# Performance work log

Measured on AMD Instinct MI355X. Metric: run time of the kernel, lower is better.

## Reference

```python
import jax, jax.numpy as jnp
import numpy as np

N_HEADS = 16


def setup_inputs() -> dict:
    key = jax.random.key(0)
    k1, k2, k3 = jax.random.split(key, 3)
    b, t, d = 2, 2048, 1024
    x = jax.random.normal(k1, (b, t, d), dtype=jnp.float32)
    # nn.Linear weights (stored here as [in, out]); 0.02 scale ~ standard init
    w_qkv = jax.random.normal(k2, (d, 3 * d), dtype=jnp.float32) * 0.02
    w_out = jax.random.normal(k3, (d, d), dtype=jnp.float32) * 0.02
    return {"x": x, "w_qkv": w_qkv, "w_out": w_out}


def reference(x, w_qkv, w_out):
    # Causal multi-head self-attention. The original module implements this
    # via a hand-rolled blockwise flash-attention loop with online softmax;
    # the intended math is exactly standard causal SDPA, expressed densely here.
    b, t, d = x.shape
    h = N_HEADS
    hd = d // h
    qkv = (x @ w_qkv).reshape(b, t, 3, h, hd)
    qkv = jnp.transpose(qkv, (2, 0, 3, 1, 4))  # [3, b, h, t, hd]
    q, k, v = qkv[0], qkv[1], qkv[2]
    scale = 1.0 / jnp.sqrt(jnp.float32(hd))
    s = jnp.einsum("bhqd,bhkd->bhqk", q, k) * scale  # [b, h, t, t]
    causal = jnp.tril(jnp.ones((t, t), dtype=bool))
    s = jnp.where(causal, s, -jnp.inf)
    p = jax.nn.softmax(s, axis=-1)
    o = jnp.einsum("bhqk,bhkd->bhqd", p, v)
    o = jnp.transpose(o, (0, 2, 1, 3)).reshape(b, t, d)
    return o @ w_out
```

## Files before the change

kernel.cpp:

```cpp
#include <hip/hip_runtime.h>

typedef float f32x4 __attribute__((ext_vector_type(4)));
typedef float f32x16 __attribute__((ext_vector_type(16)));
typedef short short8 __attribute__((ext_vector_type(8)));
typedef short short4_t __attribute__((ext_vector_type(4)));

#define GLOAD_LDS16(gp, lp) \
  __builtin_amdgcn_global_load_lds((const __attribute__((address_space(1))) void*)(gp), \
                                   (__attribute__((address_space(3))) void*)(lp), 16, 0, 0)

__device__ __forceinline__ short f2bf(float f){
  unsigned u = __builtin_bit_cast(unsigned, f);
  u += 0x7fffu + ((u >> 16) & 1u);
  return (short)(u >> 16);
}

__device__ __forceinline__ float exp2_fast(float x){
  return __builtin_amdgcn_exp2f(x);
}

__global__ void cvt_kernel(const float* __restrict__ x, short* __restrict__ xb, int n4){
  for (int i = blockIdx.x*blockDim.x + threadIdx.x; i < n4; i += gridDim.x*blockDim.x){
    f32x4 v = ((const f32x4*)x)[i];
    short4_t s;
    s[0]=f2bf(v[0]); s[1]=f2bf(v[1]); s[2]=f2bf(v[2]); s[3]=f2bf(v[3]);
    ((short4_t*)xb)[i] = s;
  }
}

__global__ __launch_bounds__(256) void transpose_cvt_kernel(const float* __restrict__ w,
                                                            short* __restrict__ wT,
                                                            int K, int N){
  __shared__ float tile[32][33];
  int bn = blockIdx.x*32, bk = blockIdx.y*32;
  int tx = threadIdx.x & 31, ty = threadIdx.x >> 5;
  #pragma unroll
  for (int r=ty; r<32; r+=8) tile[r][tx] = w[(size_t)(bk+r)*N + bn + tx];
  __syncthreads();
  #pragma unroll
  for (int r=ty; r<32; r+=8) wT[(size_t)(bn+r)*K + bk + tx] = f2bf(tile[tx][r]);
}

template<int MODE>
__global__ __launch_bounds__(256) void gemm128_kernel(
    const short* __restrict__ A, const short* __restrict__ Bt,
    float* __restrict__ Cf, short* __restrict__ qb_, short* __restrict__ kb_,
    short* __restrict__ vtb, int M, int N, int K)
{
  __shared__ short a_lds[128*64];
  __shared__ short b_lds[128*64];
  const int tid = threadIdx.x;
  const int lane = tid & 63;
  const int l15 = lane & 15, lg = lane >> 4;
  const int w  = tid >> 6;
  const int wr = w >> 1, wc = w & 1;
  const int m0 = blockIdx.x * 128, n0 = blockIdx.y * 128;

  f32x4 acc[4][4];
  #pragma unroll
  for (int i=0;i<4;i++)
    #pragma unroll
    for (int j=0;j<4;j++) acc[i][j] = (f32x4){0.f,0.f,0.f,0.f};

  for (int kt = 0; kt < K; kt += 64){
    __syncthreads();
    #pragma unroll
    for (int i=0;i<4;i++){
      int u = i*256 + tid;
      int row = u >> 3, cu = u & 7;
      int kl = ((cu ^ (row & 7)) << 3);
      GLOAD_LDS16(A + (size_t)(m0+row)*K + kt + kl, a_lds + (size_t)(i*256 + (tid & ~63))*8);
    }
    #pragma unroll
    for (int i=0;i<4;i++){
      int u = i*256 + tid;
      int row = u >> 3, cu = u & 7;
      int kl = ((cu ^ (row & 7)) << 3);
      GLOAD_LDS16(Bt + (size_t)(n0+row)*K + kt + kl, b_lds + (size_t)(i*256 + (tid & ~63))*8);
    }
    asm volatile("s_waitcnt vmcnt(0)" ::: "memory");
    __syncthreads();

    #pragma unroll
    for (int kk=0;kk<2;kk++){
      short8 af[4], bfr[4];
      #pragma unroll
      for (int mi=0;mi<4;mi++){
        int row = wr*64 + mi*16 + l15;
        int uu = ((kk*4 + lg) ^ (row & 7));
        af[mi] = *(const short8*)&a_lds[row*64 + uu*8];
      }
      #pragma unroll
      for (int ni=0;ni<4;ni++){
        int row = wc*64 + ni*16 + l15;
        int uu = ((kk*4 + lg) ^ (row & 7));
        bfr[ni] = *(const short8*)&b_lds[row*64 + uu*8];
      }
      #pragma unroll
      for (int mi=0;mi<4;mi++)
        #pragma unroll
        for (int ni=0;ni<4;ni++)
          acc[mi][ni] = __builtin_amdgcn_mfma_f32_16x16x32_bf16(af[mi], bfr[ni], acc[mi][ni], 0,0,0);
    }
  }

  #pragma unroll
  for (int mi=0;mi<4;mi++){
    #pragma unroll
    for (int ni=0;ni<4;ni++){
      int col = n0 + wc*64 + ni*16 + l15;
      #pragma unroll
      for (int r=0;r<4;r++){
        int rowg = m0 + wr*64 + mi*16 + lg*4 + r;
        float v = acc[mi][ni][r];
        if (MODE == 0){
          Cf[(size_t)rowg*N + col] = v;
        } else {
          int three = col >> 10, hh = (col >> 6) & 15, e = col & 63;
          int bb = rowg >> 11, t = rowg & 2047;
          int bh = bb*16 + hh;
          if (three == 0)      qb_[((size_t)bh*2048 + t)*64 + e] = f2bf(v * (0.125f*1.44269504f));
          else if (three == 1) kb_[((size_t)bh*2048 + t)*64 + e] = f2bf(v);
          else                 vtb[((size_t)bh*64 + e)*2048 + t] = f2bf(v);
        }
      }
    }
  }
}

__global__ __launch_bounds__(256) void attn_kernel(
    const short* __restrict__ q, const short* __restrict__ kbuf,
    const short* __restrict__ vt, short* __restrict__ ob)
{
  __shared__ short k_lds[2][128*64];
  __shared__ short v_lds[2][64*128];

  const int tid = threadIdx.x, lane = tid & 63, w = tid >> 6;
  const int l31 = lane & 31, hi = lane >> 5;
  const int qi = blockIdx.x >> 5;
  const int qb = (qi < 8) ? (15 - qi) : (qi - 8);
  const int bh = blockIdx.x & 31;
  const int q0 = qb * 128;

  const short* qg = q + ((size_t)bh*2048 + q0 + w*32 + l31)*64 + hi*8;
  short8 qf[4];
  #pragma unroll
  for (int kk=0;kk<4;kk++) qf[kk] = *(const short8*)(qg + kk*16);

  f32x16 o_acc[2];
  #pragma unroll
  for (int oc=0;oc<2;oc++)
    #pragma unroll
    for (int r=0;r<16;r++) o_acc[oc][r] = 0.f;
  float mreg = -1e30f, lreg = 0.f;

  const int sw = l31 & 7;
  int kro[4], vro[8];
  #pragma unroll
  for (int kk=0;kk<4;kk++) kro[kk] = l31*128 + (((kk*2+hi)^sw) << 4);
  #pragma unroll
  for (int ks=0;ks<8;ks++) vro[ks] = l31*256 + (((ks*2+hi)^sw) << 4);

  const int xk = ((tid & 7) ^ ((tid >> 3) & 7)) * 8;
  const int xv = ((tid & 15) ^ ((tid >> 4) & 7)) * 8;
  const short* kp = kbuf + (size_t)bh*2048*64 + (size_t)(tid >> 3)*64 + xk;
  const short* vp = vt   + (size_t)bh*64*2048 + (size_t)(tid >> 4)*2048 + xv;
  const int dst = (tid & ~63)*8;

  const int n = qb + 1;
  #pragma unroll
  for (int i=0;i<4;i++) GLOAD_LDS16(kp + i*2048,  &k_lds[0][i*2048 + dst]);
  #pragma unroll
  for (int i=0;i<4;i++) GLOAD_LDS16(vp + i*32768, &v_lds[0][i*2048 + dst]);
  kp += 8192; vp += 128;

  for (int s = 0; s < n; s++){
    const int cur = s & 1;
    if (s + 1 < n){
      #pragma unroll
      for (int i=0;i<4;i++) GLOAD_LDS16(kp + i*2048,  &k_lds[cur^1][i*2048 + dst]);
      #pragma unroll
      for (int i=0;i<4;i++) GLOAD_LDS16(vp + i*32768, &v_lds[cur^1][i*2048 + dst]);
      kp += 8192; vp += 128;
      asm volatile("s_waitcnt vmcnt(8)" ::: "memory");
    } else {
      asm volatile("s_waitcnt vmcnt(0)" ::: "memory");
    }
    __builtin_amdgcn_s_barrier();

    const char* kl_ = (const char*)&k_lds[cur][0];
    const char* vl_ = (const char*)&v_lds[cur][0];

    f32x16 sacc[4];
    #pragma unroll
    for (int ct=0;ct<4;ct++)
      #pragma unroll
      for (int r=0;r<16;r++) sacc[ct][r] = 0.f;
    __builtin_amdgcn_s_setprio(1);
    #pragma unroll
    for (int kk=0;kk<4;kk++){
      #pragma unroll
      for (int ct=0;ct<4;ct++){
        short8 kf = *(const short8*)(kl_ + kro[kk] + ct*4096);
        sacc[ct] = __builtin_amdgcn_mfma_f32_32x32x16_bf16(kf, qf[kk], sacc[ct], 0,0,0);
      }
    }
    __builtin_amdgcn_s_setprio(0);

    if (s == qb){
      const int qloc = w*32 + l31 - 4*hi;
      #pragma unroll
      for (int ct=0;ct<4;ct++)
        #pragma unroll
        for (int r=0;r<16;r++)
          if (ct*32 + (r&3) + 8*(r>>2) > qloc) sacc[ct][r] = -1e30f;
    }

    float pmax = sacc[0][0];
    #pragma unroll
    for (int ct=0;ct<4;ct++)
      #pragma unroll
      for (int r=0;r<16;r++) pmax = fmaxf(pmax, sacc[ct][r]);
    pmax = fmaxf(pmax, __shfl_xor(pmax, 32));

    if (!__all(pmax - mreg <= 8.0f)){
      float mnew = fmaxf(mreg, pmax);
      float alpha = exp2_fast(mreg - mnew);
      mreg = mnew;
      lreg *= alpha;
      float aRow[16];
      #pragma unroll
      for (int r=0;r<16;r++) aRow[r] = __shfl(alpha, (r&3) + 8*(r>>2) + 4*hi);
      #pragma unroll
      for (int oc=0;oc<2;oc++)
        #pragma unroll
        for (int r=0;r<16;r++) o_acc[oc][r] *= aRow[r];
    }

    float sum = 0.f;
    #pragma unroll
    for (int ct=0;ct<4;ct++){
      float pv[16];
      #pragma unroll
      for (int r=0;r<16;r++){ pv[r] = exp2_fast(sacc[ct][r] - mreg); sum += pv[r]; }
      unsigned pk[8];
      #pragma unroll
      for (int t=0;t<8;t++)
        asm("v_cvt_pk_bf16_f32 %0, %1, %2" : "=v"(pk[t]) : "v"(pv[2*t]), "v"(pv[2*t+1]));
      #pragma unroll
      for (int kss=0;kss<2;kss++){
        const int W = 4*kss;
        unsigned x0 = pk[W],   x2 = pk[W+2];
        unsigned x1 = pk[W+1], x3 = pk[W+3];
        asm("v_permlane32_swap_b32 %0, %1" : "+v"(x0), "+v"(x2));
        asm("v_permlane32_swap_b32 %0, %1" : "+v"(x1), "+v"(x3));
        uint4 pau = {x0, x1, x2, x3};
        short8 pa = __builtin_bit_cast(short8, pau);
        __builtin_amdgcn_s_setprio(1);
        #pragma unroll
        for (int oc=0;oc<2;oc++){
          short8 vf = *(const short8*)(vl_ + vro[2*ct+kss] + oc*8192);
          o_acc[oc] = __builtin_amdgcn_mfma_f32_32x32x16_bf16(pa, vf, o_acc[oc], 0,0,0);
        }
        __builtin_amdgcn_s_setprio(0);
      }
    }
    sum += __shfl_xor(sum, 32);
    lreg += sum;

    __builtin_amdgcn_s_barrier();
  }

  const int bb = bh >> 4, hh = bh & 15;
  #pragma unroll
  for (int r=0;r<16;r++){
    float lf = __shfl(lreg, (r&3) + 8*(r>>2) + 4*hi);
    float inv = 1.0f / lf;
    int t = q0 + w*32 + (r&3) + 8*(r>>2) + 4*hi;
    size_t base = ((size_t)(bb*2048 + t))*1024 + (size_t)hh*64 + l31;
    ob[base]      = f2bf(o_acc[0][r] * inv);
    ob[base + 32] = f2bf(o_acc[1][r] * inv);
  }
}

extern "C" void kernel_launch(void* const* d_in, const int* in_sizes, int n_in,
                              void* d_out, int out_size, void* d_ws, size_t ws_size,
                              hipStream_t stream) {
  const float* x     = (const float*)d_in[0];
  const float* w_qkv = (const float*)d_in[1];
  const float* w_out = (const float*)d_in[2];
  float* out = (float*)d_out;

  char* ws = (char*)d_ws;
  short* xb    = (short*)(ws);
  short* wqkvT = (short*)(ws + (8u  << 20));
  short* woutT = (short*)(ws + (14u << 20));
  short* qbuf  = (short*)(ws + (16u << 20));
  short* kbuf  = (short*)(ws + (24u << 20));
  short* vtbuf = (short*)(ws + (32u << 20));
  short* obuf  = (short*)(ws + (40u << 20));

  cvt_kernel<<<2048, 256, 0, stream>>>(x, xb, (4096*1024)/4);
  transpose_cvt_kernel<<<dim3(96,32), 256, 0, stream>>>(w_qkv, wqkvT, 1024, 3072);
  transpose_cvt_kernel<<<dim3(32,32), 256, 0, stream>>>(w_out, woutT, 1024, 1024);

  gemm128_kernel<1><<<dim3(32,24), 256, 0, stream>>>(xb, wqkvT, nullptr,
                                                     qbuf, kbuf, vtbuf, 4096, 3072, 1024);
  attn_kernel<<<dim3(512), 256, 0, stream>>>(qbuf, kbuf, vtbuf, obuf);
  gemm128_kernel<0><<<dim3(32,8), 256, 0, stream>>>(obuf, woutT, out,
                                                    nullptr, nullptr, nullptr, 4096, 1024, 1024);
}
```

Before: 117.2 us.

## Shrink attention KV tile from 128 to 64 keys and batch PV MFMAs

The flash-attention kernel now streams K and V in 64-key tiles instead of 128, halving LDS per buffer and doubling loop iterations. The causal mask applies to the last two tiles. PV MFMAs are deferred until all P fragments are built. Smaller LDS may allow more resident blocks per CU, and the diagonal tile does less masked work, at the cost of twice as many barriers and more per-iteration softmax overhead.

```diff
diff --git a/kernel.cpp b/kernel.cpp
--- a/kernel.cpp
+++ b/kernel.cpp
@@ -132,8 +132,8 @@
     const short* __restrict__ q, const short* __restrict__ kbuf,
     const short* __restrict__ vt, short* __restrict__ ob)
 {
-  __shared__ short k_lds[2][128*64];
-  __shared__ short v_lds[2][64*128];
+  __shared__ short k_lds[2][64*64];
+  __shared__ short v_lds[2][64*64];
 
   const int tid = threadIdx.x, lane = tid & 63, w = tid >> 6;
   const int l31 = lane & 31, hi = lane >> 5;
@@ -155,34 +155,31 @@
   float mreg = -1e30f, lreg = 0.f;
 
   const int sw = l31 & 7;
-  int kro[4], vro[8];
-  #pragma unroll
-  for (int kk=0;kk<4;kk++) kro[kk] = l31*128 + (((kk*2+hi)^sw) << 4);
-  #pragma unroll
-  for (int ks=0;ks<8;ks++) vro[ks] = l31*256 + (((ks*2+hi)^sw) << 4);
-
-  const int xk = ((tid & 7) ^ ((tid >> 3) & 7)) * 8;
-  const int xv = ((tid & 15) ^ ((tid >> 4) & 7)) * 8;
-  const short* kp = kbuf + (size_t)bh*2048*64 + (size_t)(tid >> 3)*64 + xk;
-  const short* vp = vt   + (size_t)bh*64*2048 + (size_t)(tid >> 4)*2048 + xv;
+  int ro[4];
+  #pragma unroll
+  for (int u=0;u<4;u++) ro[u] = l31*128 + (((u*2+hi)^sw) << 4);
+
+  const int xsw = ((tid & 7) ^ ((tid >> 3) & 7)) * 8;
+  const short* kp = kbuf + (size_t)bh*2048*64 + (size_t)(tid >> 3)*64   + xsw;
+  const short* vp = vt   + (size_t)bh*64*2048 + (size_t)(tid >> 3)*2048 + xsw;
   const int dst = (tid & ~63)*8;
 
-  const int n = qb + 1;
-  #pragma unroll
-  for (int i=0;i<4;i++) GLOAD_LDS16(kp + i*2048,  &k_lds[0][i*2048 + dst]);
-  #pragma unroll
-  for (int i=0;i<4;i++) GLOAD_LDS16(vp + i*32768, &v_lds[0][i*2048 + dst]);
-  kp += 8192; vp += 128;
+  const int n = 2*qb + 2;
+  #pragma unroll
+  for (int i=0;i<2;i++) GLOAD_LDS16(kp + i*2048,  &k_lds[0][i*2048 + dst]);
+  #pragma unroll
+  for (int i=0;i<2;i++) GLOAD_LDS16(vp + i*65536, &v_lds[0][i*2048 + dst]);
+  kp += 4096; vp += 64;
 
   for (int s = 0; s < n; s++){
     const int cur = s & 1;
     if (s + 1 < n){
       #pragma unroll
-      for (int i=0;i<4;i++) GLOAD_LDS16(kp + i*2048,  &k_lds[cur^1][i*2048 + dst]);
-      #pragma unroll
-      for (int i=0;i<4;i++) GLOAD_LDS16(vp + i*32768, &v_lds[cur^1][i*2048 + dst]);
-      kp += 8192; vp += 128;
-      asm volatile("s_waitcnt vmcnt(8)" ::: "memory");
+      for (int i=0;i<2;i++) GLOAD_LDS16(kp + i*2048,  &k_lds[cur^1][i*2048 + dst]);
+      #pragma unroll
+      for (int i=0;i<2;i++) GLOAD_LDS16(vp + i*65536, &v_lds[cur^1][i*2048 + dst]);
+      kp += 4096; vp += 64;
+      asm volatile("s_waitcnt vmcnt(4)" ::: "memory");
     } else {
       asm volatile("s_waitcnt vmcnt(0)" ::: "memory");
     }
@@ -191,34 +188,35 @@
     const char* kl_ = (const char*)&k_lds[cur][0];
     const char* vl_ = (const char*)&v_lds[cur][0];
 
-    f32x16 sacc[4];
-    #pragma unroll
-    for (int ct=0;ct<4;ct++)
+    f32x16 sacc[2];
+    #pragma unroll
+    for (int ct=0;ct<2;ct++)
       #pragma unroll
       for (int r=0;r<16;r++) sacc[ct][r] = 0.f;
     __builtin_amdgcn_s_setprio(1);
     #pragma unroll
     for (int kk=0;kk<4;kk++){
       #pragma unroll
-      for (int ct=0;ct<4;ct++){
-        short8 kf = *(const short8*)(kl_ + kro[kk] + ct*4096);
+      for (int ct=0;ct<2;ct++){
+        short8 kf = *(const short8*)(kl_ + ro[kk] + ct*4096);
         sacc[ct] = __builtin_amdgcn_mfma_f32_32x32x16_bf16(kf, qf[kk], sacc[ct], 0,0,0);
       }
     }
     __builtin_amdgcn_s_setprio(0);
 
-    if (s == qb){
+    if (s >= 2*qb){
+      const int d = s - 2*qb;
       const int qloc = w*32 + l31 - 4*hi;
       #pragma unroll
-      for (int ct=0;ct<4;ct++)
+      for (int ct=0;ct<2;ct++)
         #pragma unroll
         for (int r=0;r<16;r++)
-          if (ct*32 + (r&3) + 8*(r>>2) > qloc) sacc[ct][r] = -1e30f;
+          if (d*64 + ct*32 + (r&3) + 8*(r>>2) > qloc) sacc[ct][r] = -1e30f;
     }
 
     float pmax = sacc[0][0];
     #pragma unroll
-    for (int ct=0;ct<4;ct++)
+    for (int ct=0;ct<2;ct++)
       #pragma unroll
       for (int r=0;r<16;r++) pmax = fmaxf(pmax, sacc[ct][r]);
     pmax = fmaxf(pmax, __shfl_xor(pmax, 32));
@@ -238,8 +236,9 @@
     }
 
     float sum = 0.f;
-    #pragma unroll
-    for (int ct=0;ct<4;ct++){
+    short8 pa[4];
+    #pragma unroll
+    for (int ct=0;ct<2;ct++){
       float pv[16];
       #pragma unroll
       for (int r=0;r<16;r++){ pv[r] = exp2_fast(sacc[ct][r] - mreg); sum += pv[r]; }
@@ -255,18 +254,22 @@
         asm("v_permlane32_swap_b32 %0, %1" : "+v"(x0), "+v"(x2));
         asm("v_permlane32_swap_b32 %0, %1" : "+v"(x1), "+v"(x3));
         uint4 pau = {x0, x1, x2, x3};
-        short8 pa = __builtin_bit_cast(short8, pau);
-        __builtin_amdgcn_s_setprio(1);
-        #pragma unroll
-        for (int oc=0;oc<2;oc++){
-          short8 vf = *(const short8*)(vl_ + vro[2*ct+kss] + oc*8192);
-          o_acc[oc] = __builtin_amdgcn_mfma_f32_32x32x16_bf16(pa, vf, o_acc[oc], 0,0,0);
-        }
-        __builtin_amdgcn_s_setprio(0);
+        pa[2*ct+kss] = __builtin_bit_cast(short8, pau);
       }
     }
     sum += __shfl_xor(sum, 32);
     lreg += sum;
+
+    __builtin_amdgcn_s_setprio(1);
+    #pragma unroll
+    for (int ks=0;ks<4;ks++){
+      #pragma unroll
+      for (int oc=0;oc<2;oc++){
+        short8 vf = *(const short8*)(vl_ + ro[ks] + oc*4096);
+        o_acc[oc] = __builtin_amdgcn_mfma_f32_32x32x16_bf16(pa[ks], vf, o_acc[oc], 0,0,0);
+      }
+    }
+    __builtin_amdgcn_s_setprio(0);
 
     __builtin_amdgcn_s_barrier();
   }
```

Measured after the change: 124.2 us. +6.0%, slower.

## Merge prep conversions into one kernel and transpose V in a separate pass

Applied to the files above, without the earlier changes.

Fuses the x conversion and both weight transpose-conversions into a single launch that dispatches on block index. The QKV GEMM now writes V in row-major [bh,t,e] layout, and a new LDS-based transpose kernel produces V^T for attention. This replaces the GEMM epilogue's strided scatter into V^T with coalesced stores. In exchange it adds an extra launch and an extra read and write of V, and the output buffer reuses the V buffer region.

```diff
diff --git a/kernel.cpp b/kernel.cpp
--- a/kernel.cpp
+++ b/kernel.cpp
@@ -19,21 +19,31 @@
   return __builtin_amdgcn_exp2f(x);
 }
 
-__global__ void cvt_kernel(const float* __restrict__ x, short* __restrict__ xb, int n4){
-  for (int i = blockIdx.x*blockDim.x + threadIdx.x; i < n4; i += gridDim.x*blockDim.x){
-    f32x4 v = ((const f32x4*)x)[i];
-    short4_t s;
-    s[0]=f2bf(v[0]); s[1]=f2bf(v[1]); s[2]=f2bf(v[2]); s[3]=f2bf(v[3]);
-    ((short4_t*)xb)[i] = s;
-  }
-}
-
-__global__ __launch_bounds__(256) void transpose_cvt_kernel(const float* __restrict__ w,
-                                                            short* __restrict__ wT,
-                                                            int K, int N){
+__global__ __launch_bounds__(256) void prep_kernel(
+    const float* __restrict__ x, const float* __restrict__ wqkv,
+    const float* __restrict__ wout, short* __restrict__ xb,
+    short* __restrict__ wqkvT, short* __restrict__ woutT)
+{
   __shared__ float tile[32][33];
-  int bn = blockIdx.x*32, bk = blockIdx.y*32;
-  int tx = threadIdx.x & 31, ty = threadIdx.x >> 5;
+  const int bid = blockIdx.x, tid = threadIdx.x;
+  if (bid < 512){
+    int base = bid*2048 + tid;
+    #pragma unroll
+    for (int it=0; it<8; it++){
+      int i = base + it*256;
+      f32x4 v = ((const f32x4*)x)[i];
+      short4_t s;
+      s[0]=f2bf(v[0]); s[1]=f2bf(v[1]); s[2]=f2bf(v[2]); s[3]=f2bf(v[3]);
+      ((short4_t*)xb)[i] = s;
+    }
+    return;
+  }
+  const float* w; short* wT; int N, idx;
+  if (bid < 3584){ w = wqkv; wT = wqkvT; N = 3072; idx = bid - 512;  }
+  else           { w = wout; wT = woutT; N = 1024; idx = bid - 3584; }
+  const int K = 1024;
+  int bn = (idx % (N >> 5)) * 32, bk = (idx / (N >> 5)) * 32;
+  int tx = tid & 31, ty = tid >> 5;
   #pragma unroll
   for (int r=ty; r<32; r+=8) tile[r][tx] = w[(size_t)(bk+r)*N + bn + tx];
   __syncthreads();
@@ -45,7 +55,7 @@
 __global__ __launch_bounds__(256) void gemm128_kernel(
     const short* __restrict__ A, const short* __restrict__ Bt,
     float* __restrict__ Cf, short* __restrict__ qb_, short* __restrict__ kb_,
-    short* __restrict__ vtb, int M, int N, int K)
+    short* __restrict__ vb_, int M, int N, int K)
 {
   __shared__ short a_lds[128*64];
   __shared__ short b_lds[128*64];
@@ -121,11 +131,34 @@
           int bh = bb*16 + hh;
           if (three == 0)      qb_[((size_t)bh*2048 + t)*64 + e] = f2bf(v * (0.125f*1.44269504f));
           else if (three == 1) kb_[((size_t)bh*2048 + t)*64 + e] = f2bf(v);
-          else                 vtb[((size_t)bh*64 + e)*2048 + t] = f2bf(v);
+          else                 vb_[((size_t)bh*2048 + t)*64 + e] = f2bf(v);
         }
       }
     }
   }
+}
+
+__global__ __launch_bounds__(256) void transpose_v_kernel(const short* __restrict__ vb,
+                                                          short* __restrict__ vtb){
+  __shared__ short tl[64][66];
+  const int bh = blockIdx.x >> 5, t0 = (blockIdx.x & 31)*64;
+  const int r = threadIdx.x >> 2, c4 = (threadIdx.x & 3)*16;
+  const short* src = vb + ((size_t)bh*2048 + t0 + r)*64 + c4;
+  short8 a0 = *(const short8*)(src);
+  short8 a1 = *(const short8*)(src + 8);
+  #pragma unroll
+  for (int j=0;j<8;j++) tl[r][c4+j] = a0[j];
+  #pragma unroll
+  for (int j=0;j<8;j++) tl[r][c4+8+j] = a1[j];
+  __syncthreads();
+  short8 b0, b1;
+  #pragma unroll
+  for (int j=0;j<8;j++) b0[j] = tl[c4+j][r];
+  #pragma unroll
+  for (int j=0;j<8;j++) b1[j] = tl[c4+8+j][r];
+  short* dst = vtb + ((size_t)bh*64 + r)*2048 + t0 + c4;
+  *(short8*)dst = b0;
+  *(short8*)(dst+8) = b1;
 }
 
 __global__ __launch_bounds__(256) void attn_kernel(
@@ -297,15 +330,14 @@
   short* woutT = (short*)(ws + (14u << 20));
   short* qbuf  = (short*)(ws + (16u << 20));
   short* kbuf  = (short*)(ws + (24u << 20));
-  short* vtbuf = (short*)(ws + (32u << 20));
-  short* obuf  = (short*)(ws + (40u << 20));
-
-  cvt_kernel<<<2048, 256, 0, stream>>>(x, xb, (4096*1024)/4);
-  transpose_cvt_kernel<<<dim3(96,32), 256, 0, stream>>>(w_qkv, wqkvT, 1024, 3072);
-  transpose_cvt_kernel<<<dim3(32,32), 256, 0, stream>>>(w_out, woutT, 1024, 1024);
-
+  short* vbuf  = (short*)(ws + (32u << 20));
+  short* vtbuf = (short*)(ws + (40u << 20));
+  short* obuf  = vbuf;
+
+  prep_kernel<<<4608, 256, 0, stream>>>(x, w_qkv, w_out, xb, wqkvT, woutT);
   gemm128_kernel<1><<<dim3(32,24), 256, 0, stream>>>(xb, wqkvT, nullptr,
-                                                     qbuf, kbuf, vtbuf, 4096, 3072, 1024);
+                                                     qbuf, kbuf, vbuf, 4096, 3072, 1024);
+  transpose_v_kernel<<<1024, 256, 0, stream>>>(vbuf, vtbuf);
   attn_kernel<<<dim3(512), 256, 0, stream>>>(qbuf, kbuf, vtbuf, obuf);
   gemm128_kernel<0><<<dim3(32,8), 256, 0, stream>>>(obuf, woutT, out,
                                                     nullptr, nullptr, nullptr, 4096, 1024, 1024);
```

Result: no change. 115.4 us (-1.6%).
